# Performance work log

Hardware: AMD Instinct MI355X
Metric: run time of the kernel (lower is better)

The kernel has to match this reference:

```python
import jax, jax.numpy as jnp
import numpy as np

B = 32768    # number of trees (batch)
N = 10       # nodes per tree (forced by Linear(embed_dim*10, ...))
L = 10       # leaf tokens per subtree (also 10, same cat constraint)
E = 16       # embed_dim
H = 8        # hidden_dim
V = 2000     # embed_dict_size
LAT = 128    # latent_vector_dim
EPS = 1e-5   # BatchNorm1d eps


def setup_inputs() -> dict:
    key = jax.random.key(0)
    ks = jax.random.split(key, 17)
    w = lambda k, shape, s=0.05: (jax.random.normal(k, shape, jnp.float32) * s)
    return {
        "tokens": jax.random.randint(ks[0], (B, N, L), 0, V),
        "emb":    w(ks[1], (V, E), 0.1),            # nn.Embedding weight
        "w_ih":   w(ks[2], (4 * E, E)),             # LSTM input weights (i,f,g,o)
        "b_ih":   w(ks[3], (4 * E,)),
        "b_hh":   w(ks[4], (4 * E,)),               # h0=c0=0 so W_hh never contributes
        "ffW1":   w(ks[5], (4 * E, 10 * E)),        # child_sum_ff Linear(160,64)
        "ffb1":   w(ks[6], (4 * E,)),
        "ffW2":   w(ks[7], (E, 4 * E)),             # child_sum_ff Linear(64,16)
        "ffb2":   w(ks[8], (E,)),
        "fmW":    w(ks[9], (H, E)),                 # ff_model Linear(16,8)
        "fmb":    w(ks[10], (H,)),
        "tsW":    w(ks[11], (1, H)),                # tail_score Linear(8,1)
        "tsb":    w(ks[12], (1,)),
        "suW":    w(ks[13], (LAT, H)),              # tail_summary Linear(8,latent)
        "sub_b":  w(ks[14], (LAT,)),
        "gamma":  jnp.ones((LAT,), jnp.float32),    # BatchNorm1d affine
        "beta":   jnp.zeros((LAT,), jnp.float32),
    }


def _child_ff(x, W1, b1, W2, b2):
    # nn.Sequential(Linear(160,64), ReLU, Linear(64,16))
    return jax.nn.relu(x @ W1.T + b1) @ W2.T + b2


def _lstm_single_step(x, w_ih, b_ih, b_hh):
    # One-timestep LSTM with zero initial (h, c); PyTorch gate order i,f,g,o.
    gates = x @ w_ih.T + b_ih + b_hh
    i, f, g, o = jnp.split(gates, 4, axis=-1)
    c = jax.nn.sigmoid(i) * jnp.tanh(g)          # f * c0 = 0
    return jax.nn.sigmoid(o) * jnp.tanh(c)


def reference(tokens, emb, w_ih, b_ih, b_hh, ffW1, ffb1, ffW2, ffb2,
              fmW, fmb, tsW, tsb, suW, sub_b, gamma, beta):
    leaf = emb[tokens]                                        # (B,N,L,E) gather
    subtree = _child_ff(leaf.reshape(B, N, L * E),
                        ffW1, ffb1, ffW2, ffb2)               # (B,N,E)
    h = _lstm_single_step(subtree, w_ih, b_ih, b_hh)          # (B,N,E)
    code = _child_ff(h.reshape(B, N * E), ffW1, ffb1, ffW2, ffb2)  # (B,E)
    ff_out = code @ fmW.T + fmb                               # (B,H)
    score = jnp.tanh(ff_out @ tsW.T + tsb)                    # (B,1)
    s = ff_out @ suW.T + sub_b                                # (B,LAT)
    mu = jnp.mean(s, axis=0)
    var = jnp.var(s, axis=0)                                  # biased, training-mode BN
    summary = gamma * (s - mu) / jnp.sqrt(var + EPS) + beta
    return score, summary
```

## Files before the change

### kernel.cpp

```cpp
#include <hip/hip_runtime.h>
#include <hip/hip_bf16.h>

#define BB 32768
#define NN 10
#define VV 2000
#define EPSBN 1e-5

__global__ __launch_bounds__(256) void k_table(const float* __restrict__ emb,
                                               const float* __restrict__ W1,
                                               float* __restrict__ T1) {
  int idx = blockIdx.x * 256 + threadIdx.x;
  if (idx >= VV * 640) return;
  int v = idx / 640;
  int r = idx - v * 640;
  int l = r >> 6;
  int o = r & 63;
  const float* e = emb + v * 16;
  const float* w = W1 + o * 160 + l * 16;
  float s = 0.f;
#pragma unroll
  for (int k = 0; k < 16; ++k) s = fmaf(e[k], w[k], s);
  T1[idx] = s;
}

__global__ __launch_bounds__(256) void k_fuse(const float* __restrict__ w_ih,
    const float* __restrict__ b_ih, const float* __restrict__ b_hh,
    const float* __restrict__ W2, const float* __restrict__ b2v,
    float* __restrict__ W3T, float* __restrict__ bias3T) {
  int idx = blockIdx.x * 256 + threadIdx.x;
  if (idx < 3072) {
    int k = idx / 48, jj = idx - k * 48;
    int gr = (jj < 16) ? jj : jj + 16;
    float s = 0.f;
#pragma unroll
    for (int o = 0; o < 16; ++o) s = fmaf(w_ih[gr * 16 + o], W2[o * 64 + k], s);
    W3T[idx] = s;
  } else if (idx < 3120) {
    int jj = idx - 3072;
    int gr = (jj < 16) ? jj : jj + 16;
    float s = b_ih[gr] + b_hh[gr];
#pragma unroll
    for (int o = 0; o < 16; ++o) s = fmaf(w_ih[gr * 16 + o], b2v[o], s);
    bias3T[jj] = s;
  }
}

__global__ __attribute__((amdgpu_waves_per_eu(2, 3)))
__launch_bounds__(256) void k_stage1(const int* __restrict__ tokens,
    const float* __restrict__ T1, const float* __restrict__ b1v,
    const float* __restrict__ W3T_and_bias,
    float* __restrict__ hbuf) {
  __shared__ __align__(16) float w_lds[3120];
  const int tid = threadIdx.x;
  for (int i = tid; i < 780; i += 256)
    ((float4*)w_lds)[i] = ((const float4*)W3T_and_bias)[i];

  const int item = blockIdx.x * 256 + tid;
  int tk[10];
  {
    const int2* tp2 = (const int2*)(tokens + (size_t)item * 10);
#pragma unroll
    for (int q = 0; q < 5; ++q) { int2 t = tp2[q]; tk[2 * q] = t.x; tk[2 * q + 1] = t.y; }
  }
  __syncthreads();

  float4 h[16];
  {
    const float4* r = (const float4*)(T1 + (size_t)tk[0] * 640);
#pragma unroll
    for (int c = 0; c < 16; ++c) h[c] = r[c];
  }
#pragma unroll
  for (int l = 1; l < 10; ++l) {
    const float4* r = (const float4*)(T1 + (size_t)tk[l] * 640 + l * 64);
#pragma unroll
    for (int c = 0; c < 16; ++c) {
      float4 v = r[c];
      h[c].x += v.x; h[c].y += v.y; h[c].z += v.z; h[c].w += v.w;
    }
  }
  float h1[64];
  {
    const float4* b1q = (const float4*)b1v;
#pragma unroll
    for (int c = 0; c < 16; ++c) {
      float4 bq = b1q[c];
      h1[4 * c]     = fmaxf(h[c].x + bq.x, 0.f);
      h1[4 * c + 1] = fmaxf(h[c].y + bq.y, 0.f);
      h1[4 * c + 2] = fmaxf(h[c].z + bq.z, 0.f);
      h1[4 * c + 3] = fmaxf(h[c].w + bq.w, 0.f);
    }
  }

  float acc[48];
#pragma unroll
  for (int j4 = 0; j4 < 12; ++j4) {
    float4 b = *(const float4*)&w_lds[3072 + j4 * 4];
    acc[4 * j4] = b.x; acc[4 * j4 + 1] = b.y; acc[4 * j4 + 2] = b.z; acc[4 * j4 + 3] = b.w;
  }
#pragma unroll
  for (int k = 0; k < 64; ++k) {
    const float hk = h1[k];
#pragma unroll
    for (int j4 = 0; j4 < 12; ++j4) {
      float4 w = *(const float4*)&w_lds[k * 48 + j4 * 4];
      acc[4 * j4]     = fmaf(w.x, hk, acc[4 * j4]);
      acc[4 * j4 + 1] = fmaf(w.y, hk, acc[4 * j4 + 1]);
      acc[4 * j4 + 2] = fmaf(w.z, hk, acc[4 * j4 + 2]);
      acc[4 * j4 + 3] = fmaf(w.w, hk, acc[4 * j4 + 3]);
    }
  }

  float res[16];
#pragma unroll
  for (int j = 0; j < 16; ++j) {
    float si = __builtin_amdgcn_rcpf(1.f + __expf(-acc[j]));
    float tg = fmaf(2.f, __builtin_amdgcn_rcpf(1.f + __expf(-2.f * acc[16 + j])), -1.f);
    float so = __builtin_amdgcn_rcpf(1.f + __expf(-acc[32 + j]));
    float c = si * tg;
    float th = fmaf(2.f, __builtin_amdgcn_rcpf(1.f + __expf(-2.f * c)), -1.f);
    res[j] = so * th;
  }
  float4* op = (float4*)(hbuf + (size_t)item * 16);
#pragma unroll
  for (int q = 0; q < 4; ++q)
    op[q] = make_float4(res[4 * q], res[4 * q + 1], res[4 * q + 2], res[4 * q + 3]);
}

__global__ __launch_bounds__(256) void k_stage2(const float* __restrict__ hbuf,
    const float* __restrict__ W1, const float* __restrict__ b1v,
    const float* __restrict__ W2, const float* __restrict__ b2v,
    const float* __restrict__ fmW, const float* __restrict__ fmb,
    const float* __restrict__ tsW, const float* __restrict__ tsb,
    const float* __restrict__ suW, const float* __restrict__ sub_b,
    float* __restrict__ out, float* __restrict__ partials) {
  __shared__ float h1b_lds[32 * 68];
  __shared__ float code_lds[32 * 20];
  __shared__ float ff_lds[32 * 12];
  int tid = threadIdx.x;
  int lane = tid & 63;
  int wid = __builtin_amdgcn_readfirstlane(tid >> 6);
  int treeBase = blockIdx.x * 32;
  {
    int tw = treeBase + wid * 8;
    float acc[8];
#pragma unroll
    for (int t = 0; t < 8; ++t) acc[t] = b1v[lane];
    const float* wrow = W1 + lane * 160;
    const float* xbase = hbuf + (size_t)tw * 160;
    for (int k = 0; k < 160; k += 4) {
      float4 wv = *(const float4*)(wrow + k);
#pragma unroll
      for (int t = 0; t < 8; ++t) {
        float4 xv = *(const float4*)(xbase + t * 160 + k);
        acc[t] = fmaf(wv.x, xv.x, acc[t]);
        acc[t] = fmaf(wv.y, xv.y, acc[t]);
        acc[t] = fmaf(wv.z, xv.z, acc[t]);
        acc[t] = fmaf(wv.w, xv.w, acc[t]);
      }
    }
#pragma unroll
    for (int t = 0; t < 8; ++t)
      h1b_lds[(wid * 8 + t) * 68 + lane] = fmaxf(acc[t], 0.f);
  }
  __syncthreads();
  {
    int t2 = tid >> 3, jj = tid & 7;
    float c0 = b2v[jj], c1 = b2v[jj + 8];
    const float* w2a = W2 + jj * 64;
    const float* w2b = W2 + (jj + 8) * 64;
    const float* hb = &h1b_lds[t2 * 68];
    for (int o = 0; o < 64; o += 4) {
      float4 hv = *(const float4*)(hb + o);
      float4 a4 = *(const float4*)(w2a + o);
      float4 b4 = *(const float4*)(w2b + o);
      c0 = fmaf(a4.x, hv.x, c0); c0 = fmaf(a4.y, hv.y, c0);
      c0 = fmaf(a4.z, hv.z, c0); c0 = fmaf(a4.w, hv.w, c0);
      c1 = fmaf(b4.x, hv.x, c1); c1 = fmaf(b4.y, hv.y, c1);
      c1 = fmaf(b4.z, hv.z, c1); c1 = fmaf(b4.w, hv.w, c1);
    }
    code_lds[t2 * 20 + jj] = c0;
    code_lds[t2 * 20 + jj + 8] = c1;
  }
  __syncthreads();
  {
    int t = tid >> 3, q = tid & 7;
    float f = fmb[q];
    const float* cw = fmW + q * 16;
    const float* cl = &code_lds[t * 20];
#pragma unroll
    for (int j4 = 0; j4 < 16; j4 += 4) {
      float4 cv = *(const float4*)(cl + j4);
      float4 wv = *(const float4*)(cw + j4);
      f = fmaf(wv.x, cv.x, f); f = fmaf(wv.y, cv.y, f);
      f = fmaf(wv.z, cv.z, f); f = fmaf(wv.w, cv.w, f);
    }
    ff_lds[t * 12 + q] = f;
  }
  __syncthreads();
  {
    int t = tid >> 3, r = tid & 7;
    float4 f0 = *(const float4*)&ff_lds[t * 12];
    float4 f1 = *(const float4*)&ff_lds[t * 12 + 4];
    int tree = treeBase + t;
    float* od = out + (size_t)BB + (size_t)tree * 128 + r * 16;
#pragma unroll
    for (int cc = 0; cc < 16; ++cc) {
      int c = r * 16 + cc;
      const float* u = suW + c * 8;
      float4 u0 = *(const float4*)(u);
      float4 u1 = *(const float4*)(u + 4);
      float sv = sub_b[c];
      sv = fmaf(u0.x, f0.x, sv); sv = fmaf(u0.y, f0.y, sv);
      sv = fmaf(u0.z, f0.z, sv); sv = fmaf(u0.w, f0.w, sv);
      sv = fmaf(u1.x, f1.x, sv); sv = fmaf(u1.y, f1.y, sv);
      sv = fmaf(u1.z, f1.z, sv); sv = fmaf(u1.w, f1.w, sv);
      od[cc] = sv;
    }
    if (tid < 32) {
      int tt = tid;
      float4 g0 = *(const float4*)&ff_lds[tt * 12];
      float4 g1 = *(const float4*)&ff_lds[tt * 12 + 4];
      float sc = tsb[0];
      sc = fmaf(tsW[0], g0.x, sc); sc = fmaf(tsW[1], g0.y, sc);
      sc = fmaf(tsW[2], g0.z, sc); sc = fmaf(tsW[3], g0.w, sc);
      sc = fmaf(tsW[4], g1.x, sc); sc = fmaf(tsW[5], g1.y, sc);
      sc = fmaf(tsW[6], g1.z, sc); sc = fmaf(tsW[7], g1.w, sc);
      out[treeBase + tt] = tanhf(sc);
    }
  }
  {
    int waveId = blockIdx.x * 4 + wid;
    float* pw = partials + (size_t)waveId * 88;
#pragma unroll
    for (int rep = 0; rep < 2; ++rep) {
      int e = lane + rep * 64;
      if (e < 81) {
        int i = e / 9, jx = e - i * 9;
        float m = 0.f;
#pragma unroll
        for (int t = 0; t < 8; ++t) {
          const float* fr = &ff_lds[(wid * 8 + t) * 12];
          float fi = (i  < 8) ? fr[i]  : 1.f;
          float fj = (jx < 8) ? fr[jx] : 1.f;
          m = fmaf(fi, fj, m);
        }
        pw[e] = m;
      }
    }
  }
}

__global__ __launch_bounds__(256) void k_reduce(const float* __restrict__ partials,
                                                double* __restrict__ Msum) {
  __shared__ double red[256];
  int e = blockIdx.x;
  double s = 0.0;
  for (int w = threadIdx.x; w < 4096; w += 256)
    s += (double)partials[(size_t)w * 88 + e];
  red[threadIdx.x] = s;
  __syncthreads();
  for (int off = 128; off > 0; off >>= 1) {
    if (threadIdx.x < off) red[threadIdx.x] += red[threadIdx.x + off];
    __syncthreads();
  }
  if (threadIdx.x == 0) Msum[e] = red[0];
}

__global__ __launch_bounds__(128) void k_stats(const double* __restrict__ Msum,
    const float* __restrict__ suW, const float* __restrict__ sub_b,
    const float* __restrict__ gamma, const float* __restrict__ beta,
    float* __restrict__ statsA, float* __restrict__ statsB) {
  int c = threadIdx.x;
  double u[9];
#pragma unroll
  for (int q = 0; q < 8; ++q) u[q] = (double)suW[c * 8 + q];
  u[8] = (double)sub_b[c];
  double S1 = 0.0;
#pragma unroll
  for (int i = 0; i < 9; ++i) S1 += u[i] * Msum[72 + i];
  double mu = S1 / (double)BB;
  double E2 = 0.0;
#pragma unroll
  for (int i = 0; i < 9; ++i) {
    double acc = 0.0;
#pragma unroll
    for (int jx = 0; jx < 9; ++jx) acc += u[jx] * Msum[i * 9 + jx];
    E2 += u[i] * acc;
  }
  E2 /= (double)BB;
  double var = E2 - mu * mu;
  if (var < 0.0) var = 0.0;
  double rs = 1.0 / sqrt(var + (double)EPSBN);
  double A = (double)gamma[c] * rs;
  statsA[c] = (float)A;
  statsB[c] = (float)((double)beta[c] - mu * A);
}

__global__ __launch_bounds__(256) void k_norm(float* __restrict__ out,
    const float* __restrict__ statsA, const float* __restrict__ statsB) {
  int idx = blockIdx.x * 256 + threadIdx.x;
  float4* p = (float4*)(out + BB);
  float4 v = p[idx];
  int c4 = idx & 31;
  float4 a = ((const float4*)statsA)[c4];
  float4 b = ((const float4*)statsB)[c4];
  v.x = fmaf(v.x, a.x, b.x);
  v.y = fmaf(v.y, a.y, b.y);
  v.z = fmaf(v.z, a.z, b.z);
  v.w = fmaf(v.w, a.w, b.w);
  p[idx] = v;
}

extern "C" void kernel_launch(void* const* d_in, const int* in_sizes, int n_in,
                              void* d_out, int out_size, void* d_ws, size_t ws_size,
                              hipStream_t stream) {
  const int*   tokens = (const int*)d_in[0];
  const float* emb   = (const float*)d_in[1];
  const float* w_ih  = (const float*)d_in[2];
  const float* b_ih  = (const float*)d_in[3];
  const float* b_hh  = (const float*)d_in[4];
  const float* ffW1  = (const float*)d_in[5];
  const float* ffb1  = (const float*)d_in[6];
  const float* ffW2  = (const float*)d_in[7];
  const float* ffb2  = (const float*)d_in[8];
  const float* fmW   = (const float*)d_in[9];
  const float* fmb   = (const float*)d_in[10];
  const float* tsW   = (const float*)d_in[11];
  const float* tsb   = (const float*)d_in[12];
  const float* suW   = (const float*)d_in[13];
  const float* sub_b = (const float*)d_in[14];
  const float* gamma = (const float*)d_in[15];
  const float* beta  = (const float*)d_in[16];
  float* out = (float*)d_out;
  float* ws = (float*)d_ws;

  float*  T1       = ws;
  float*  hbuf     = T1 + 1280000;
  float*  partials = hbuf + 5242880;
  double* Msum     = (double*)(partials + 360448);
  float*  statsA   = (float*)(Msum + 82);
  float*  statsB   = statsA + 128;
  float*  W3T      = statsB + 128;
  float*  bias3T   = W3T + 3072;

  hipLaunchKernelGGL(k_table,  dim3(5000), dim3(256), 0, stream, emb, ffW1, T1);
  hipLaunchKernelGGL(k_fuse,   dim3(13),   dim3(256), 0, stream,
                     w_ih, b_ih, b_hh, ffW2, ffb2, W3T, bias3T);
  hipLaunchKernelGGL(k_stage1, dim3(1280), dim3(256), 0, stream,
                     tokens, T1, ffb1, W3T, hbuf);
  hipLaunchKernelGGL(k_stage2, dim3(1024), dim3(256), 0, stream,
                     hbuf, ffW1, ffb1, ffW2, ffb2, fmW, fmb, tsW, tsb, suW, sub_b,
                     out, partials);
  hipLaunchKernelGGL(k_reduce, dim3(81),   dim3(256), 0, stream, partials, Msum);
  hipLaunchKernelGGL(k_stats,  dim3(1),    dim3(128), 0, stream,
                     Msum, suW, sub_b, gamma, beta, statsA, statsB);
  hipLaunchKernelGGL(k_norm,   dim3(4096), dim3(256), 0, stream, out, statsA, statsB);
}
```

Measured before the change: 223.1 us.

## Process two items per thread in stage1, merge prep kernels, fold bias into table

Stage1 now handles two (tree,node) items per thread, so each LDS weight float4 read feeds two sets of FMAs. The gather-and-accumulate is chunked by 16 hidden units to limit live registers, and the grid is halved. The table and weight-fusion prep kernels are merged into one launch, and the first-layer bias is folded into the table's l=0 slice so stage1 no longer adds it. The register budget grows and occupancy is pinned at 2 waves/EU, which may cut latency hiding for the random gathers.

After: 262.4 us. +17.6%, slower.

```diff
diff --git a/kernel.cpp b/kernel.cpp
--- a/kernel.cpp
+++ b/kernel.cpp
@@ -6,48 +6,47 @@
 #define VV 2000
 #define EPSBN 1e-5
 
-__global__ __launch_bounds__(256) void k_table(const float* __restrict__ emb,
-                                               const float* __restrict__ W1,
-                                               float* __restrict__ T1) {
-  int idx = blockIdx.x * 256 + threadIdx.x;
-  if (idx >= VV * 640) return;
-  int v = idx / 640;
-  int r = idx - v * 640;
-  int l = r >> 6;
-  int o = r & 63;
-  const float* e = emb + v * 16;
-  const float* w = W1 + o * 160 + l * 16;
-  float s = 0.f;
-#pragma unroll
-  for (int k = 0; k < 16; ++k) s = fmaf(e[k], w[k], s);
-  T1[idx] = s;
-}
-
-__global__ __launch_bounds__(256) void k_fuse(const float* __restrict__ w_ih,
-    const float* __restrict__ b_ih, const float* __restrict__ b_hh,
-    const float* __restrict__ W2, const float* __restrict__ b2v,
-    float* __restrict__ W3T, float* __restrict__ bias3T) {
-  int idx = blockIdx.x * 256 + threadIdx.x;
-  if (idx < 3072) {
-    int k = idx / 48, jj = idx - k * 48;
-    int gr = (jj < 16) ? jj : jj + 16;
-    float s = 0.f;
-#pragma unroll
-    for (int o = 0; o < 16; ++o) s = fmaf(w_ih[gr * 16 + o], W2[o * 64 + k], s);
-    W3T[idx] = s;
-  } else if (idx < 3120) {
-    int jj = idx - 3072;
-    int gr = (jj < 16) ? jj : jj + 16;
-    float s = b_ih[gr] + b_hh[gr];
-#pragma unroll
-    for (int o = 0; o < 16; ++o) s = fmaf(w_ih[gr * 16 + o], b2v[o], s);
-    bias3T[jj] = s;
-  }
-}
-
-__global__ __attribute__((amdgpu_waves_per_eu(2, 3)))
+__global__ __launch_bounds__(256) void k_prep(const float* __restrict__ emb,
+    const float* __restrict__ W1, const float* __restrict__ b1v,
+    const float* __restrict__ w_ih, const float* __restrict__ b_ih,
+    const float* __restrict__ b_hh, const float* __restrict__ W2,
+    const float* __restrict__ b2v,
+    float* __restrict__ T1, float* __restrict__ W3T, float* __restrict__ bias3T) {
+  if (blockIdx.x < 5000) {
+    int idx = blockIdx.x * 256 + threadIdx.x;
+    int v = idx / 640;
+    int r = idx - v * 640;
+    int l = r >> 6;
+    int o = r & 63;
+    const float* e = emb + v * 16;
+    const float* w = W1 + o * 160 + l * 16;
+    float s = (l == 0) ? b1v[o] : 0.f;
+#pragma unroll
+    for (int k = 0; k < 16; ++k) s = fmaf(e[k], w[k], s);
+    T1[idx] = s;
+  } else {
+    int idx = (blockIdx.x - 5000) * 256 + threadIdx.x;
+    if (idx < 3072) {
+      int k = idx / 48, jj = idx - k * 48;
+      int gr = (jj < 16) ? jj : jj + 16;
+      float s = 0.f;
+#pragma unroll
+      for (int o = 0; o < 16; ++o) s = fmaf(w_ih[gr * 16 + o], W2[o * 64 + k], s);
+      W3T[idx] = s;
+    } else if (idx < 3120) {
+      int jj = idx - 3072;
+      int gr = (jj < 16) ? jj : jj + 16;
+      float s = b_ih[gr] + b_hh[gr];
+#pragma unroll
+      for (int o = 0; o < 16; ++o) s = fmaf(w_ih[gr * 16 + o], b2v[o], s);
+      bias3T[jj] = s;
+    }
+  }
+}
+
+__global__ __attribute__((amdgpu_waves_per_eu(2, 2)))
 __launch_bounds__(256) void k_stage1(const int* __restrict__ tokens,
-    const float* __restrict__ T1, const float* __restrict__ b1v,
+    const float* __restrict__ T1,
     const float* __restrict__ W3T_and_bias,
     float* __restrict__ hbuf) {
   __shared__ __align__(16) float w_lds[3120];
@@ -55,76 +54,111 @@
   for (int i = tid; i < 780; i += 256)
     ((float4*)w_lds)[i] = ((const float4*)W3T_and_bias)[i];
 
-  const int item = blockIdx.x * 256 + tid;
-  int tk[10];
-  {
-    const int2* tp2 = (const int2*)(tokens + (size_t)item * 10);
-#pragma unroll
-    for (int q = 0; q < 5; ++q) { int2 t = tp2[q]; tk[2 * q] = t.x; tk[2 * q + 1] = t.y; }
-  }
-  __syncthreads();
-
-  float4 h[16];
-  {
-    const float4* r = (const float4*)(T1 + (size_t)tk[0] * 640);
-#pragma unroll
-    for (int c = 0; c < 16; ++c) h[c] = r[c];
-  }
-#pragma unroll
-  for (int l = 1; l < 10; ++l) {
-    const float4* r = (const float4*)(T1 + (size_t)tk[l] * 640 + l * 64);
-#pragma unroll
-    for (int c = 0; c < 16; ++c) {
-      float4 v = r[c];
-      h[c].x += v.x; h[c].y += v.y; h[c].z += v.z; h[c].w += v.w;
-    }
-  }
-  float h1[64];
-  {
-    const float4* b1q = (const float4*)b1v;
-#pragma unroll
-    for (int c = 0; c < 16; ++c) {
-      float4 bq = b1q[c];
-      h1[4 * c]     = fmaxf(h[c].x + bq.x, 0.f);
-      h1[4 * c + 1] = fmaxf(h[c].y + bq.y, 0.f);
-      h1[4 * c + 2] = fmaxf(h[c].z + bq.z, 0.f);
-      h1[4 * c + 3] = fmaxf(h[c].w + bq.w, 0.f);
-    }
-  }
-
-  float acc[48];
+  const int i0 = blockIdx.x * 512 + tid;
+  const int i1 = i0 + 256;
+  int tk0[10], tk1[10];
+  {
+    const int2* p = (const int2*)(tokens + (size_t)i0 * 10);
+#pragma unroll
+    for (int q = 0; q < 5; ++q) { int2 t = p[q]; tk0[2 * q] = t.x; tk0[2 * q + 1] = t.y; }
+  }
+  {
+    const int2* p = (const int2*)(tokens + (size_t)i1 * 10);
+#pragma unroll
+    for (int q = 0; q < 5; ++q) { int2 t = p[q]; tk1[2 * q] = t.x; tk1[2 * q + 1] = t.y; }
+  }
+  __syncthreads();
+
+  float acc0[48], acc1[48];
 #pragma unroll
   for (int j4 = 0; j4 < 12; ++j4) {
-    float4 b = *(const float4*)&w_lds[3072 + j4 * 4];
-    acc[4 * j4] = b.x; acc[4 * j4 + 1] = b.y; acc[4 * j4 + 2] = b.z; acc[4 * j4 + 3] = b.w;
-  }
-#pragma unroll
-  for (int k = 0; k < 64; ++k) {
-    const float hk = h1[k];
-#pragma unroll
-    for (int j4 = 0; j4 < 12; ++j4) {
-      float4 w = *(const float4*)&w_lds[k * 48 + j4 * 4];
-      acc[4 * j4]     = fmaf(w.x, hk, acc[4 * j4]);
-      acc[4 * j4 + 1] = fmaf(w.y, hk, acc[4 * j4 + 1]);
-      acc[4 * j4 + 2] = fmaf(w.z, hk, acc[4 * j4 + 2]);
-      acc[4 * j4 + 3] = fmaf(w.w, hk, acc[4 * j4 + 3]);
-    }
-  }
-
-  float res[16];
-#pragma unroll
-  for (int j = 0; j < 16; ++j) {
-    float si = __builtin_amdgcn_rcpf(1.f + __expf(-acc[j]));
-    float tg = fmaf(2.f, __builtin_amdgcn_rcpf(1.f + __expf(-2.f * acc[16 + j])), -1.f);
-    float so = __builtin_amdgcn_rcpf(1.f + __expf(-acc[32 + j]));
-    float c = si * tg;
-    float th = fmaf(2.f, __builtin_amdgcn_rcpf(1.f + __expf(-2.f * c)), -1.f);
-    res[j] = so * th;
-  }
-  float4* op = (float4*)(hbuf + (size_t)item * 16);
-#pragma unroll
-  for (int q = 0; q < 4; ++q)
-    op[q] = make_float4(res[4 * q], res[4 * q + 1], res[4 * q + 2], res[4 * q + 3]);
+    float4 b = *(const float4*)&w_lds[3072 + 4 * j4];
+    acc0[4 * j4] = b.x; acc0[4 * j4 + 1] = b.y; acc0[4 * j4 + 2] = b.z; acc0[4 * j4 + 3] = b.w;
+    acc1[4 * j4] = b.x; acc1[4 * j4 + 1] = b.y; acc1[4 * j4 + 2] = b.z; acc1[4 * j4 + 3] = b.w;
+  }
+
+#pragma unroll
+  for (int c = 0; c < 4; ++c) {
+    float4 q0[4], q1[4];
+    {
+      const float4* r0 = (const float4*)(T1 + (size_t)tk0[0] * 640 + c * 16);
+      const float4* r1 = (const float4*)(T1 + (size_t)tk1[0] * 640 + c * 16);
+#pragma unroll
+      for (int u = 0; u < 4; ++u) { q0[u] = r0[u]; q1[u] = r1[u]; }
+    }
+#pragma unroll
+    for (int l = 1; l < 10; ++l) {
+      const float4* r0 = (const float4*)(T1 + (size_t)tk0[l] * 640 + l * 64 + c * 16);
+      const float4* r1 = (const float4*)(T1 + (size_t)tk1[l] * 640 + l * 64 + c * 16);
+#pragma unroll
+      for (int u = 0; u < 4; ++u) {
+        float4 v0 = r0[u], v1 = r1[u];
+        q0[u].x += v0.x; q0[u].y += v0.y; q0[u].z += v0.z; q0[u].w += v0.w;
+        q1[u].x += v1.x; q1[u].y += v1.y; q1[u].z += v1.z; q1[u].w += v1.w;
+      }
+    }
+    float h0[16], h1c[16];
+#pragma unroll
+    for (int u = 0; u < 4; ++u) {
+      h0[4 * u]     = fmaxf(q0[u].x, 0.f);
+      h0[4 * u + 1] = fmaxf(q0[u].y, 0.f);
+      h0[4 * u + 2] = fmaxf(q0[u].z, 0.f);
+      h0[4 * u + 3] = fmaxf(q0[u].w, 0.f);
+      h1c[4 * u]     = fmaxf(q1[u].x, 0.f);
+      h1c[4 * u + 1] = fmaxf(q1[u].y, 0.f);
+      h1c[4 * u + 2] = fmaxf(q1[u].z, 0.f);
+      h1c[4 * u + 3] = fmaxf(q1[u].w, 0.f);
+    }
+#pragma unroll
+    for (int k = 0; k < 16; ++k) {
+      const float x0 = h0[k], x1 = h1c[k];
+#pragma unroll
+      for (int j4 = 0; j4 < 12; ++j4) {
+        float4 w = *(const float4*)&w_lds[(c * 16 + k) * 48 + 4 * j4];
+        acc0[4 * j4]     = fmaf(w.x, x0, acc0[4 * j4]);
+        acc0[4 * j4 + 1] = fmaf(w.y, x0, acc0[4 * j4 + 1]);
+        acc0[4 * j4 + 2] = fmaf(w.z, x0, acc0[4 * j4 + 2]);
+        acc0[4 * j4 + 3] = fmaf(w.w, x0, acc0[4 * j4 + 3]);
+        acc1[4 * j4]     = fmaf(w.x, x1, acc1[4 * j4]);
+        acc1[4 * j4 + 1] = fmaf(w.y, x1, acc1[4 * j4 + 1]);
+        acc1[4 * j4 + 2] = fmaf(w.z, x1, acc1[4 * j4 + 2]);
+        acc1[4 * j4 + 3] = fmaf(w.w, x1, acc1[4 * j4 + 3]);
+      }
+    }
+  }
+
+  {
+    float res[16];
+#pragma unroll
+    for (int j = 0; j < 16; ++j) {
+      float si = __builtin_amdgcn_rcpf(1.f + __expf(-acc0[j]));
+      float tg = fmaf(2.f, __builtin_amdgcn_rcpf(1.f + __expf(-2.f * acc0[16 + j])), -1.f);
+      float so = __builtin_amdgcn_rcpf(1.f + __expf(-acc0[32 + j]));
+      float cc = si * tg;
+      float th = fmaf(2.f, __builtin_amdgcn_rcpf(1.f + __expf(-2.f * cc)), -1.f);
+      res[j] = so * th;
+    }
+    float4* op = (float4*)(hbuf + (size_t)i0 * 16);
+#pragma unroll
+    for (int q = 0; q < 4; ++q)
+      op[q] = make_float4(res[4 * q], res[4 * q + 1], res[4 * q + 2], res[4 * q + 3]);
+  }
+  {
+    float res[16];
+#pragma unroll
+    for (int j = 0; j < 16; ++j) {
+      float si = __builtin_amdgcn_rcpf(1.f + __expf(-acc1[j]));
+      float tg = fmaf(2.f, __builtin_amdgcn_rcpf(1.f + __expf(-2.f * acc1[16 + j])), -1.f);
+      float so = __builtin_amdgcn_rcpf(1.f + __expf(-acc1[32 + j]));
+      float cc = si * tg;
+      float th = fmaf(2.f, __builtin_amdgcn_rcpf(1.f + __expf(-2.f * cc)), -1.f);
+      res[j] = so * th;
+    }
+    float4* op = (float4*)(hbuf + (size_t)i1 * 16);
+#pragma unroll
+    for (int q = 0; q < 4; ++q)
+      op[q] = make_float4(res[4 * q], res[4 * q + 1], res[4 * q + 2], res[4 * q + 3]);
+  }
 }
 
 __global__ __launch_bounds__(256) void k_stage2(const float* __restrict__ hbuf,
@@ -344,11 +378,10 @@
   float*  W3T      = statsB + 128;
   float*  bias3T   = W3T + 3072;
 
-  hipLaunchKernelGGL(k_table,  dim3(5000), dim3(256), 0, stream, emb, ffW1, T1);
-  hipLaunchKernelGGL(k_fuse,   dim3(13),   dim3(256), 0, stream,
-                     w_ih, b_ih, b_hh, ffW2, ffb2, W3T, bias3T);
-  hipLaunchKernelGGL(k_stage1, dim3(1280), dim3(256), 0, stream,
-                     tokens, T1, ffb1, W3T, hbuf);
+  hipLaunchKernelGGL(k_prep,   dim3(5013), dim3(256), 0, stream,
+                     emb, ffW1, ffb1, w_ih, b_ih, b_hh, ffW2, ffb2, T1, W3T, bias3T);
+  hipLaunchKernelGGL(k_stage1, dim3(640),  dim3(256), 0, stream,
+                     tokens, T1, W3T, hbuf);
   hipLaunchKernelGGL(k_stage2, dim3(1024), dim3(256), 0, stream,
                      hbuf, ffW1, ffb1, ffW2, ffb2, fmW, fmb, tsW, tsb, suW, sub_b,
                      out, partials);
```
